# Optimization experiments

Measured on AMD Instinct MI355X. Metric: run time of the kernel, lower is better.

## Reference

```python
import jax, jax.numpy as jnp
import numpy as np

C = 512
C8 = C // 8
B, H, W = 4, 64, 64


def _conv1x1(x, w, b):
    # x: (B, Cin, H, W), w: (Cout, Cin), b: (Cout,)
    return jnp.einsum('oi,bihw->bohw', w, x) + b[None, :, None, None]


def setup_inputs() -> dict:
    key = jax.random.key(0)
    ks = jax.random.split(key, 16)
    s = 0.02
    inp = {
        'x': jax.random.normal(ks[0], (B, C, H, W), dtype=jnp.float32),
        'wpq': jax.random.normal(ks[1], (C8, C), dtype=jnp.float32) * s,
        'bpq': jnp.zeros((C8,), jnp.float32),
        'wpk': jax.random.normal(ks[2], (C8, C), dtype=jnp.float32) * s,
        'bpk': jnp.zeros((C8,), jnp.float32),
        'wpv': jax.random.normal(ks[3], (C, C), dtype=jnp.float32) * s,
        'bpv': jnp.zeros((C,), jnp.float32),
        'wcq': jax.random.normal(ks[4], (C, C), dtype=jnp.float32) * s,
        'bcq': jnp.zeros((C,), jnp.float32),
        'wck': jax.random.normal(ks[5], (C, C), dtype=jnp.float32) * s,
        'bck': jnp.zeros((C,), jnp.float32),
        'wcv': jax.random.normal(ks[6], (C, C), dtype=jnp.float32) * s,
        'bcv': jnp.zeros((C,), jnp.float32),
        # gammas are zero-init in torch; use small nonzero values so both
        # attention branches contribute to the output numerically.
        'gpos': jax.random.normal(ks[7], (1,), dtype=jnp.float32) * 0.1,
        'gchan': jax.random.normal(ks[8], (1,), dtype=jnp.float32) * 0.1,
    }
    return inp


def reference(x, wpq, bpq, wpk, bpk, wpv, bpv, wcq, bcq, wck, bck, wcv, bcv, gpos, gchan):
    b, c, h, w = x.shape
    n = h * w
    # ---- position attention ----
    pos_q = _conv1x1(x, wpq, bpq).reshape(b, C8, n)           # (b, C/8, N)
    pos_k = _conv1x1(x, wpk, bpk).reshape(b, C8, n)           # (b, C/8, N)
    pos_v = _conv1x1(x, wpv, bpv).reshape(b, c, n)            # (b, C, N)
    pos_attn = jax.nn.softmax(jnp.einsum('bcq,bck->bqk', pos_q, pos_k), axis=-1)  # (b, N, N)
    pos_out = jnp.einsum('bck,bqk->bcq', pos_v, pos_attn).reshape(b, c, h, w)
    pos_out = gpos * pos_out + x
    # ---- channel attention ----
    chan_q = _conv1x1(pos_out, wcq, bcq).reshape(b, c, n)
    chan_k = _conv1x1(pos_out, wck, bck).reshape(b, c, n)
    chan_v = _conv1x1(pos_out, wcv, bcv).reshape(b, c, n)
    chan_attn = jax.nn.softmax(jnp.einsum('bin,bjn->bij', chan_q, chan_k), axis=-1)  # (b, C, C)
    chan_out = jnp.einsum('bij,bjn->bin', chan_attn, chan_v).reshape(b, c, h, w)
    return gchan * chan_out + pos_out
```

## Files before the change

kernel.cpp:

```cpp
#include <hip/hip_runtime.h>
#include <hip/hip_bf16.h>
#include <math.h>

typedef __bf16 bf16;
typedef __attribute__((ext_vector_type(8))) __bf16 bf16x8;
typedef __attribute__((ext_vector_type(4))) __bf16 bf16x4;
typedef __attribute__((ext_vector_type(4))) float f32x4;

#define DEVI static __device__ __forceinline__

DEVI int swzb(int row, int ch) { return ((ch ^ (row & 7)) << 4); }

DEVI void gl_lds16(const void* g, void* l) {
  __builtin_amdgcn_global_load_lds(
      (const __attribute__((address_space(1))) unsigned int*)g,
      (__attribute__((address_space(3))) unsigned int*)l, 16, 0, 0);
}

__global__ __launch_bounds__(256) void prep_weights(
    const float* __restrict__ wpq, const float* __restrict__ wpk,
    const float* __restrict__ wpv, const float* __restrict__ wcq,
    const float* __restrict__ wck, const float* __restrict__ wcv,
    const float* __restrict__ bpq, const float* __restrict__ bpk,
    bf16* __restrict__ wqk, bf16* __restrict__ wpvb, bf16* __restrict__ wcqb,
    bf16* __restrict__ wckb, bf16* __restrict__ wcvT, float* __restrict__ bqk)
{
  int i = blockIdx.x * 256 + threadIdx.x;
  switch (blockIdx.y) {
    case 0: if (i < 64*512)  wqk[i]          = (bf16)wpq[i]; break;
    case 1: if (i < 64*512)  wqk[64*512 + i] = (bf16)wpk[i]; break;
    case 2: if (i < 512*512) wpvb[i] = (bf16)wpv[i]; break;
    case 3: if (i < 512*512) wcqb[i] = (bf16)wcq[i]; break;
    case 4: if (i < 512*512) wckb[i] = (bf16)wck[i]; break;
    case 5: if (i < 512*512) { int t = i >> 9, j = i & 511; wcvT[i] = (bf16)wcv[j*512 + t]; } break;
    case 6: if (i < 64) bqk[i] = bpq[i]; else if (i < 128) bqk[i] = bpk[i - 64]; break;
  }
}

__global__ __launch_bounds__(256) void transpose_x(const float* __restrict__ x, bf16* __restrict__ xbT)
{
  __shared__ float t[32][33];
  int b = blockIdx.z, n0 = blockIdx.x * 32, c0 = blockIdx.y * 32;
  int tx = threadIdx.x & 31, ty = threadIdx.x >> 5;
#pragma unroll
  for (int i = 0; i < 4; ++i)
    t[ty + 8*i][tx] = x[((size_t)b*512 + c0 + ty + 8*i)*4096 + n0 + tx];
  __syncthreads();
#pragma unroll
  for (int i = 0; i < 4; ++i)
    xbT[((size_t)b*4096 + n0 + ty + 8*i)*512 + c0 + tx] = (bf16)t[tx][ty + 8*i];
}

struct GemmP {
  const bf16* A; const bf16* Bt; void* C;
  long aS, bS;
  long cSbytes;
  int lda, ldb, ldc, K;
  const float* biasM; const float* biasN;
  const float* e_bq; const float* e_v; const float* e_u; const float* e_bk; float e_nn;
  long vS, uS;
  const float* gchan; const float* Abv; const bf16* Pres; long abvS, presS;
};

template<int BM, int BN, int BIAS, int EPI>
__global__ __launch_bounds__(256) void gemm_k(GemmP p)
{
  constexpr int QF = BM / 32;
  constexpr int CF = BN / 32;
  __shared__ __align__(16) char sa[2][BM * 128];
  __shared__ __align__(16) char sb[2][BN * 128];
  const int tid = threadIdx.x, lane = tid & 63, w = tid >> 6;
  const int g = lane >> 4, l15 = lane & 15;
  const int bm = blockIdx.x * BM, bn = blockIdx.y * BN, bz = blockIdx.z;
  const bf16* A  = p.A  + (size_t)bz * p.aS;
  const bf16* Bt = p.Bt + (size_t)bz * p.bS;
  char* Cb = (char*)p.C + (size_t)bz * p.cSbytes;
  const int wm = (w & 1) * (BM / 2), wn = (w >> 1) * (BN / 2);
  const int srow = tid >> 3, sch = tid & 7;

  f32x4 acc[QF][CF];
#pragma unroll
  for (int i = 0; i < QF; ++i)
#pragma unroll
    for (int j = 0; j < CF; ++j) acc[i][j] = f32x4{0.f, 0.f, 0.f, 0.f};

  auto stage = [&](int k0, int bi) {
#pragma unroll
    for (int it = 0; it < BM / 32; ++it) {
      int r = it * 32 + srow;
      gl_lds16(A + (size_t)(bm + r) * p.lda + k0 + ((sch ^ (r & 7)) * 8),
               sa[bi] + (it * 32 + w * 8) * 128);
    }
#pragma unroll
    for (int it = 0; it < BN / 32; ++it) {
      int r = it * 32 + srow;
      gl_lds16(Bt + (size_t)(bn + r) * p.ldb + k0 + ((sch ^ (r & 7)) * 8),
               sb[bi] + (it * 32 + w * 8) * 128);
    }
  };

  stage(0, 0);
  __syncthreads();
  const int nk = p.K >> 6;
  for (int t = 0; t < nk; ++t) {
    const int cur = t & 1;
    if (t + 1 < nk) stage((t + 1) << 6, cur ^ 1);
#pragma unroll
    for (int kc = 0; kc < 2; ++kc) {
      bf16x8 af[QF], bfr[CF];
#pragma unroll
      for (int qf = 0; qf < QF; ++qf) {
        int row = wm + 16 * qf + l15;
        af[qf] = *(const bf16x8*)(sa[cur] + row * 128 + swzb(row, g + 4 * kc));
      }
#pragma unroll
      for (int cf = 0; cf < CF; ++cf) {
        int row = wn + 16 * cf + l15;
        bfr[cf] = *(const bf16x8*)(sb[cur] + row * 128 + swzb(row, g + 4 * kc));
      }
      __builtin_amdgcn_s_setprio(1);
#pragma unroll
      for (int qf = 0; qf < QF; ++qf)
#pragma unroll
        for (int cf = 0; cf < CF; ++cf)
          acc[qf][cf] = __builtin_amdgcn_mfma_f32_16x16x32_bf16(af[qf], bfr[cf], acc[qf][cf], 0, 0, 0);
      __builtin_amdgcn_s_setprio(0);
    }
    __syncthreads();
  }

  float gc = 0.f;
  const float* AbvB = nullptr; const bf16* PresB = nullptr;
  const float* eV = nullptr; const float* eU = nullptr;
  if (EPI == 3) { gc = p.gchan[0]; AbvB = p.Abv + (size_t)bz * p.abvS; PresB = p.Pres + (size_t)bz * p.presS; }
  if (EPI == 2) { eV = p.e_v + (size_t)bz * p.vS; eU = p.e_u + (size_t)bz * p.uS; }

#pragma unroll
  for (int qf = 0; qf < QF; ++qf)
#pragma unroll
    for (int cf = 0; cf < CF; ++cf)
#pragma unroll
      for (int r = 0; r < 4; ++r) {
        int m = bm + wm + 16 * qf + 4 * g + r;
        int n = bn + wn + 16 * cf + l15;
        float v = acc[qf][cf][r];
        if (BIAS == 1) v += p.biasM[m];
        if (BIAS == 2) v += p.biasN[n];
        size_t idx = (size_t)m * p.ldc + n;
        if (EPI == 0) ((bf16*)Cb)[idx] = (bf16)v;
        else if (EPI == 1) ((float*)Cb)[idx] = v;
        else if (EPI == 2) {
          v += p.e_bq[m] * eV[n] + eU[m] * p.e_bk[n] + p.e_nn * p.e_bq[m] * p.e_bk[n];
          ((float*)Cb)[idx] = v;
        } else {
          v = gc * (v + AbvB[m]) + (float)PresB[idx];
          ((float*)Cb)[idx] = v;
        }
      }
}

__global__ __launch_bounds__(512, 4) void flash_pos(
    const bf16* __restrict__ QKT, const bf16* __restrict__ Vv,
    const float* __restrict__ x, const float* __restrict__ gpos,
    bf16* __restrict__ Pb, bf16* __restrict__ PTb)
{
  extern __shared__ char sm[];
  char* Plds = sm + 16384;
  float* Och  = (float*)sm;
  float* lsum = (float*)(sm + 34816);

  const int tid = threadIdx.x, lane = tid & 63, w = tid >> 6;
  const int g = lane >> 4, l15 = lane & 15;
  const int wq = w & 3;
  const int wh = w >> 2;
  const int phys = blockIdx.x;
  const int b  = (phys & 7) >> 1;
  const int ch = phys & 1;
  const int q0 = (phys >> 3) << 6;
  const int c0 = ch << 8;

  const bf16* QKTb = QKT + (size_t)b * 4096 * 128;
  const bf16* Vb   = Vv  + (size_t)b * 512 * 4096;

  const bf16* qrow = QKTb + (size_t)(q0 + 16 * wq + l15) * 128;
  bf16x8 qa0 = *(const bf16x8*)(qrow + 8 * g);
  bf16x8 qa1 = *(const bf16x8*)(qrow + 32 + 8 * g);

  f32x4 acc[4][2];
#pragma unroll
  for (int i = 0; i < 4; ++i) { acc[i][0] = f32x4{0.f,0.f,0.f,0.f}; acc[i][1] = f32x4{0.f,0.f,0.f,0.f}; }
  f32x4 l_r = f32x4{0.f, 0.f, 0.f, 0.f};

  const int srow = tid >> 3, sch = tid & 7;
  const bf16* Ksrc = QKTb + (size_t)srow * 128 + 64 + ((sch ^ (srow & 7)) * 8);
  const bf16* vb0 = Vb + (size_t)(c0 + 32 * w + l15) * 4096 + g * 8;
  const bf16* vb1 = vb0 + (size_t)16 * 4096;

  bf16x8 vA[2][2], vB[2][2];

  auto subiter = [&](const char* Kcur, char* Knext, int ktn,
                     bf16x8 (&vC)[2][2], bf16x8 (&vN)[2][2]) {
    gl_lds16(Ksrc + (size_t)ktn * 8192, Knext + w * 1024);
    __builtin_amdgcn_sched_barrier(0);
#pragma unroll
    for (int kc = 0; kc < 2; ++kc) {
      vN[kc][0] = *(const bf16x8*)(vb0 + ktn * 64 + kc * 32);
      vN[kc][1] = *(const bf16x8*)(vb1 + ktn * 64 + kc * 32);
    }
    f32x4 s0 = f32x4{0.f,0.f,0.f,0.f}, s1 = f32x4{0.f,0.f,0.f,0.f};
    {
      const int r0 = 32 * wh + l15, r1 = r0 + 16;
      bf16x8 k00 = *(const bf16x8*)(Kcur + r0 * 128 + swzb(r0, g));
      bf16x8 k01 = *(const bf16x8*)(Kcur + r0 * 128 + swzb(r0, g + 4));
      bf16x8 k10 = *(const bf16x8*)(Kcur + r1 * 128 + swzb(r1, g));
      bf16x8 k11 = *(const bf16x8*)(Kcur + r1 * 128 + swzb(r1, g + 4));
      s0 = __builtin_amdgcn_mfma_f32_16x16x32_bf16(qa0, k00, s0, 0, 0, 0);
      s0 = __builtin_amdgcn_mfma_f32_16x16x32_bf16(qa1, k01, s0, 0, 0, 0);
      s1 = __builtin_amdgcn_mfma_f32_16x16x32_bf16(qa0, k10, s1, 0, 0, 0);
      s1 = __builtin_amdgcn_mfma_f32_16x16x32_bf16(qa1, k11, s1, 0, 0, 0);
    }
#pragma unroll
    for (int r = 0; r < 4; ++r) {
      float e0 = __expf(s0[r]), e1 = __expf(s1[r]);
      l_r[r] += e0 + e1;
      int row = 16 * wq + 4 * g + r;
      int ca = 32 * wh + l15, cb = ca + 16;
      *(bf16*)(Plds + row * 128 + (((ca >> 3) ^ (row & 7)) << 4) + ((ca & 7) * 2)) = (bf16)e0;
      *(bf16*)(Plds + row * 128 + (((cb >> 3) ^ (row & 7)) << 4) + ((cb & 7) * 2)) = (bf16)e1;
    }
    asm volatile("s_waitcnt lgkmcnt(0)" ::: "memory");
    __builtin_amdgcn_sched_barrier(0);
    __builtin_amdgcn_s_barrier();
    __builtin_amdgcn_sched_barrier(0);
    __builtin_amdgcn_s_setprio(1);
#pragma unroll
    for (int kc = 0; kc < 2; ++kc)
#pragma unroll
      for (int qf = 0; qf < 4; ++qf) {
        int row = 16 * qf + l15;
        bf16x8 ap = *(const bf16x8*)(Plds + row * 128 + swzb(row, g + 4 * kc));
        acc[qf][0] = __builtin_amdgcn_mfma_f32_16x16x32_bf16(ap, vC[kc][0], acc[qf][0], 0, 0, 0);
        acc[qf][1] = __builtin_amdgcn_mfma_f32_16x16x32_bf16(ap, vC[kc][1], acc[qf][1], 0, 0, 0);
      }
    __builtin_amdgcn_s_setprio(0);
    asm volatile("s_waitcnt vmcnt(4) lgkmcnt(0)" ::: "memory");
    __builtin_amdgcn_sched_barrier(0);
    __builtin_amdgcn_s_barrier();
    __builtin_amdgcn_sched_barrier(0);
  };

  gl_lds16(Ksrc, sm + w * 1024);
  __builtin_amdgcn_sched_barrier(0);
#pragma unroll
  for (int kc = 0; kc < 2; ++kc) {
    vA[kc][0] = *(const bf16x8*)(vb0 + kc * 32);
    vA[kc][1] = *(const bf16x8*)(vb1 + kc * 32);
  }
  asm volatile("s_waitcnt vmcnt(4)" ::: "memory");
  __builtin_amdgcn_sched_barrier(0);
  __builtin_amdgcn_s_barrier();
  __builtin_amdgcn_sched_barrier(0);

  for (int t = 0; t < 64; t += 2) {
    subiter(sm,        sm + 8192, (t + 1) & 63, vA, vB);
    subiter(sm + 8192, sm,        (t + 2) & 63, vB, vA);
  }
  asm volatile("s_waitcnt vmcnt(0) lgkmcnt(0)" ::: "memory");
  __builtin_amdgcn_sched_barrier(0);
  __builtin_amdgcn_s_barrier();
  __builtin_amdgcn_sched_barrier(0);

#pragma unroll
  for (int off = 1; off < 16; off <<= 1) {
#pragma unroll
    for (int r = 0; r < 4; ++r) l_r[r] += __shfl_xor(l_r[r], off);
  }
  if (l15 == 0)
#pragma unroll
    for (int r = 0; r < 4; ++r) lsum[wh * 64 + 16 * wq + 4 * g + r] = l_r[r];
  __syncthreads();

  const float gp = gpos[0];
  for (int j = 0; j < 2; ++j) {
    if ((w >> 2) == j) {
#pragma unroll
      for (int qf = 0; qf < 4; ++qf) {
        float inv[4];
#pragma unroll
        for (int r = 0; r < 4; ++r) {
          int qi = 16 * qf + 4 * g + r;
          inv[r] = gp / (lsum[qi] + lsum[64 + qi]);
        }
#pragma unroll
        for (int cf = 0; cf < 2; ++cf) {
          int cl = 32 * (w & 3) + 16 * cf + l15;
#pragma unroll
          for (int r = 0; r < 4; ++r)
            Och[cl * 68 + 16 * qf + 4 * g + r] = acc[qf][cf][r] * inv[r];
        }
      }
    }
    __syncthreads();
    {
      int cl = tid >> 2, qs = (tid & 3) * 16;
      int cg = c0 + 128 * j + cl;
      const float* xr = x + ((size_t)b * 512 + cg) * 4096 + q0 + qs;
      float* och = Och + cl * 68 + qs;
      float tmp[16];
#pragma unroll
      for (int i = 0; i < 16; ++i) { tmp[i] = och[i] + xr[i]; och[i] = tmp[i]; }
      bf16x8 o0, o1;
#pragma unroll
      for (int i = 0; i < 8; ++i) { o0[i] = (bf16)tmp[i]; o1[i] = (bf16)tmp[i + 8]; }
      bf16* pr = Pb + ((size_t)b * 512 + cg) * 4096 + q0 + qs;
      *(bf16x8*)pr = o0; *(bf16x8*)(pr + 8) = o1;
    }
    __syncthreads();
    {
      int q = tid >> 3, cs = (tid & 7) * 16;
      float tmp[16];
#pragma unroll
      for (int i = 0; i < 16; ++i) tmp[i] = Och[(cs + i) * 68 + q];
      bf16x8 o0, o1;
#pragma unroll
      for (int i = 0; i < 8; ++i) { o0[i] = (bf16)tmp[i]; o1[i] = (bf16)tmp[i + 8]; }
      bf16* pt = PTb + ((size_t)b * 4096 + q0 + q) * 512 + c0 + 128 * j + cs;
      *(bf16x8*)pt = o0; *(bf16x8*)(pt + 8) = o1;
    }
    __syncthreads();
  }
}

__global__ __launch_bounds__(256) void row_sum(const bf16* __restrict__ Pb, float* __restrict__ r)
{
  int wid = blockIdx.x * 4 + (threadIdx.x >> 6);
  int lane = threadIdx.x & 63;
  const bf16* row = Pb + (size_t)wid * 4096;
  float s = 0.f;
#pragma unroll
  for (int i = 0; i < 8; ++i) {
    bf16x8 v = ((const bf16x8*)row)[lane + 64 * i];
#pragma unroll
    for (int j = 0; j < 8; ++j) s += (float)v[j];
  }
#pragma unroll
  for (int off = 1; off < 64; off <<= 1) s += __shfl_xor(s, off);
  if (lane == 0) r[wid] = s;
}

__global__ __launch_bounds__(256) void uv_kernel(
    const float* __restrict__ wcq, const float* __restrict__ wck,
    const float* __restrict__ r, float* __restrict__ u, float* __restrict__ v)
{
  int b = blockIdx.z;
  int i = blockIdx.x * 256 + threadIdx.x;
  const float* rb = r + b * 512;
  const float* wrow = (blockIdx.y ? wck : wcq) + (size_t)i * 512;
  float s = 0.f;
  for (int t = 0; t < 512; ++t) s += wrow[t] * rb[t];
  (blockIdx.y ? v : u)[b * 512 + i] = s;
}

__global__ __launch_bounds__(256) void softmax_chan(
    const float* __restrict__ L, const float* __restrict__ bcv,
    bf16* __restrict__ Ab, float* __restrict__ Abv)
{
  int b = blockIdx.z;
  int i = blockIdx.x * 4 + (threadIdx.x >> 6);
  int lane = threadIdx.x & 63;
  const float* row = L + ((size_t)b * 512 + i) * 512;
  f32x4 v0 = ((const f32x4*)row)[lane];
  f32x4 v1 = ((const f32x4*)row)[lane + 64];
  float mx = fmaxf(fmaxf(fmaxf(v0[0], v0[1]), fmaxf(v0[2], v0[3])),
                   fmaxf(fmaxf(v1[0], v1[1]), fmaxf(v1[2], v1[3])));
#pragma unroll
  for (int off = 1; off < 64; off <<= 1) mx = fmaxf(mx, __shfl_xor(mx, off));
  float e[8]; float s = 0.f;
#pragma unroll
  for (int k = 0; k < 4; ++k) { e[k] = __expf(v0[k] - mx); s += e[k]; }
#pragma unroll
  for (int k = 0; k < 4; ++k) { e[4 + k] = __expf(v1[k] - mx); s += e[4 + k]; }
#pragma unroll
  for (int off = 1; off < 64; off <<= 1) s += __shfl_xor(s, off);
  float inv = 1.f / s;
  bf16x4 a0, a1;
  const f32x4 bv0 = ((const f32x4*)bcv)[lane];
  const f32x4 bv1 = ((const f32x4*)bcv)[lane + 64];
  float pb = 0.f;
#pragma unroll
  for (int k = 0; k < 4; ++k) {
    float p0 = e[k] * inv, p1 = e[4 + k] * inv;
    a0[k] = (bf16)p0; a1[k] = (bf16)p1;
    pb += p0 * bv0[k] + p1 * bv1[k];
  }
  bf16* arow = Ab + ((size_t)b * 512 + i) * 512;
  *(bf16x4*)(arow + 4 * lane) = a0;
  *(bf16x4*)(arow + 256 + 4 * lane) = a1;
#pragma unroll
  for (int off = 1; off < 64; off <<= 1) pb += __shfl_xor(pb, off);
  if (lane == 0) Abv[b * 512 + i] = pb;
}

extern "C" void kernel_launch(void* const* d_in, const int* in_sizes, int n_in,
                              void* d_out, int out_size, void* d_ws, size_t ws_size,
                              hipStream_t stream)
{
  const float* x    = (const float*)d_in[0];
  const float* wpq  = (const float*)d_in[1];
  const float* bpq  = (const float*)d_in[2];
  const float* wpk  = (const float*)d_in[3];
  const float* bpk  = (const float*)d_in[4];
  const float* wpv  = (const float*)d_in[5];
  const float* bpv  = (const float*)d_in[6];
  const float* wcq  = (const float*)d_in[7];
  const float* bcq  = (const float*)d_in[8];
  const float* wck  = (const float*)d_in[9];
  const float* bck  = (const float*)d_in[10];
  const float* wcv  = (const float*)d_in[11];
  const float* bcv  = (const float*)d_in[12];
  const float* gpos = (const float*)d_in[13];
  const float* gch  = (const float*)d_in[14];
  float* out = (float*)d_out;

  char* ws = (char*)d_ws;
  size_t off = 0;
  auto alloc = [&](size_t bytes) -> char* {
    char* p = ws + off; off = (off + bytes + 255) & ~(size_t)255; return p;
  };
  bf16*  xbT  = (bf16*)alloc(4UL * 4096 * 512 * 2);
  bf16*  QKT  = (bf16*)alloc(4UL * 4096 * 128 * 2);
  bf16*  V    = (bf16*)alloc(4UL * 512 * 4096 * 2);
  bf16*  Pb   = (bf16*)alloc(4UL * 512 * 4096 * 2);
  bf16*  PTb  = (bf16*)alloc(4UL * 4096 * 512 * 2);
  bf16*  G    = (bf16*)alloc(4UL * 512 * 512 * 2);
  bf16*  M1   = (bf16*)alloc(4UL * 512 * 512 * 2);
  float* Lws  = (float*)alloc(4UL * 512 * 512 * 4);
  bf16*  Ab   = (bf16*)alloc(4UL * 512 * 512 * 2);
  bf16*  B2   = (bf16*)alloc(4UL * 512 * 512 * 2);
  bf16*  wqk  = (bf16*)alloc(128UL * 512 * 2);
  bf16*  wpvb = (bf16*)alloc(512UL * 512 * 2);
  bf16*  wcqb = (bf16*)alloc(512UL * 512 * 2);
  bf16*  wckb = (bf16*)alloc(512UL * 512 * 2);
  bf16*  wcvT = (bf16*)alloc(512UL * 512 * 2);
  float* bqk  = (float*)alloc(128 * 4);
  float* rws  = (float*)alloc(4UL * 512 * 4);
  float* uws  = (float*)alloc(4UL * 512 * 4);
  float* vws  = (float*)alloc(4UL * 512 * 4);
  float* Abv  = (float*)alloc(4UL * 512 * 4);
  if (off > ws_size) return;

  prep_weights<<<dim3(1024, 7, 1), 256, 0, stream>>>(wpq, wpk, wpv, wcq, wck, wcv,
                                                     bpq, bpk, wqk, wpvb, wcqb, wckb, wcvT, bqk);
  transpose_x<<<dim3(128, 16, 4), 256, 0, stream>>>(x, xbT);

  GemmP p{};
  p = GemmP{};
  p.A = xbT; p.aS = 4096L * 512; p.lda = 512;
  p.Bt = wqk; p.bS = 0; p.ldb = 512;
  p.C = QKT; p.cSbytes = 4096L * 128 * 2; p.ldc = 128;
  p.K = 512; p.biasN = bqk;
  gemm_k<128, 64, 2, 0><<<dim3(32, 2, 4), 256, 0, stream>>>(p);

  p = GemmP{};
  p.A = wpvb; p.aS = 0; p.lda = 512;
  p.Bt = xbT; p.bS = 4096L * 512; p.ldb = 512;
  p.C = V; p.cSbytes = 512L * 4096 * 2; p.ldc = 4096;
  p.K = 512; p.biasM = bpv;
  gemm_k<128, 128, 1, 0><<<dim3(4, 32, 4), 256, 0, stream>>>(p);

  flash_pos<<<dim3(512, 1, 1), 512, 35328, stream>>>(QKT, V, x, gpos, Pb, PTb);

  p = GemmP{};
  p.A = Pb; p.aS = 512L * 4096; p.lda = 4096;
  p.Bt = Pb; p.bS = 512L * 4096; p.ldb = 4096;
  p.C = G; p.cSbytes = 512L * 512 * 2; p.ldc = 512;
  p.K = 4096;
  gemm_k<64, 64, 0, 0><<<dim3(8, 8, 4), 256, 0, stream>>>(p);

  row_sum<<<dim3(512, 1, 1), 256, 0, stream>>>(Pb, rws);
  uv_kernel<<<dim3(2, 2, 4), 256, 0, stream>>>(wcq, wck, rws, uws, vws);

  p = GemmP{};
  p.A = wcqb; p.aS = 0; p.lda = 512;
  p.Bt = G; p.bS = 512L * 512; p.ldb = 512;
  p.C = M1; p.cSbytes = 512L * 512 * 2; p.ldc = 512;
  p.K = 512;
  gemm_k<64, 64, 0, 0><<<dim3(8, 8, 4), 256, 0, stream>>>(p);

  p = GemmP{};
  p.A = M1; p.aS = 512L * 512; p.lda = 512;
  p.Bt = wckb; p.bS = 0; p.ldb = 512;
  p.C = Lws; p.cSbytes = 512L * 512 * 4; p.ldc = 512;
  p.K = 512;
  p.e_bq = bcq; p.e_v = vws; p.vS = 512; p.e_u = uws; p.uS = 512; p.e_bk = bck; p.e_nn = 4096.f;
  gemm_k<64, 64, 0, 2><<<dim3(8, 8, 4), 256, 0, stream>>>(p);

  softmax_chan<<<dim3(128, 1, 4), 256, 0, stream>>>(Lws, bcv, Ab, Abv);

  p = GemmP{};
  p.A = Ab; p.aS = 512L * 512; p.lda = 512;
  p.Bt = wcvT; p.bS = 0; p.ldb = 512;
  p.C = B2; p.cSbytes = 512L * 512 * 2; p.ldc = 512;
  p.K = 512;
  gemm_k<64, 64, 0, 0><<<dim3(8, 8, 4), 256, 0, stream>>>(p);

  p = GemmP{};
  p.A = B2; p.aS = 512L * 512; p.lda = 512;
  p.Bt = PTb; p.bS = 4096L * 512; p.ldb = 512;
  p.C = out; p.cSbytes = 512L * 4096 * 4; p.ldc = 4096;
  p.K = 512;
  p.gchan = gch; p.Abv = Abv; p.abvS = 512; p.Pres = Pb; p.presS = 512L * 4096;
  gemm_k<128, 128, 0, 3><<<dim3(4, 32, 4), 256, 0, stream>>>(p);
}
```

Baseline: 303.0 us.

## Triple-buffer GEMM staging and double-buffer P tile in flash_pos

The GEMM kernel moves to a three-stage LDS ring for small tiles (BM+BN<=192). It prefetches two K-steps ahead and waits on explicit vmcnt counts, so only one barrier is needed per iteration. In flash_pos the P tile now alternates between two LDS buffers keyed to the K buffer, which removes one of the two barriers per sub-iteration. This cuts synchronisation stalls but uses more LDS, which may lower occupancy. It also depends on the vmcnt counts being exact for correctness.

New measurement: 304.2 us. No clear change (+0.4%).

```diff
diff --git a/kernel.cpp b/kernel.cpp
--- a/kernel.cpp
+++ b/kernel.cpp
@@ -15,6 +15,18 @@
   __builtin_amdgcn_global_load_lds(
       (const __attribute__((address_space(1))) unsigned int*)g,
       (__attribute__((address_space(3))) unsigned int*)l, 16, 0, 0);
+}
+
+template<int N> DEVI void wait_vm() {
+  if constexpr (N == 0) asm volatile("s_waitcnt vmcnt(0)" ::: "memory");
+  else if constexpr (N == 4) asm volatile("s_waitcnt vmcnt(4)" ::: "memory");
+  else if constexpr (N == 6) asm volatile("s_waitcnt vmcnt(6)" ::: "memory");
+  else if constexpr (N == 8) asm volatile("s_waitcnt vmcnt(8)" ::: "memory");
+}
+DEVI void sbar() {
+  __builtin_amdgcn_sched_barrier(0);
+  __builtin_amdgcn_s_barrier();
+  __builtin_amdgcn_sched_barrier(0);
 }
 
 __global__ __launch_bounds__(256) void prep_weights(
@@ -67,8 +79,10 @@
 {
   constexpr int QF = BM / 32;
   constexpr int CF = BN / 32;
-  __shared__ __align__(16) char sa[2][BM * 128];
-  __shared__ __align__(16) char sb[2][BN * 128];
+  constexpr int NBUF = (BM + BN <= 192) ? 3 : 2;
+  constexpr int LOADS = (BM + BN) / 32;
+  __shared__ __align__(16) char sa[NBUF][BM * 128];
+  __shared__ __align__(16) char sb[NBUF][BN * 128];
   const int tid = threadIdx.x, lane = tid & 63, w = tid >> 6;
   const int g = lane >> 4, l15 = lane & 15;
   const int bm = blockIdx.x * BM, bn = blockIdx.y * BN, bz = blockIdx.z;
@@ -98,25 +112,19 @@
                sb[bi] + (it * 32 + w * 8) * 128);
     }
   };
-
-  stage(0, 0);
-  __syncthreads();
-  const int nk = p.K >> 6;
-  for (int t = 0; t < nk; ++t) {
-    const int cur = t & 1;
-    if (t + 1 < nk) stage((t + 1) << 6, cur ^ 1);
+  auto compute = [&](int bi) {
 #pragma unroll
     for (int kc = 0; kc < 2; ++kc) {
       bf16x8 af[QF], bfr[CF];
 #pragma unroll
       for (int qf = 0; qf < QF; ++qf) {
         int row = wm + 16 * qf + l15;
-        af[qf] = *(const bf16x8*)(sa[cur] + row * 128 + swzb(row, g + 4 * kc));
+        af[qf] = *(const bf16x8*)(sa[bi] + row * 128 + swzb(row, g + 4 * kc));
       }
 #pragma unroll
       for (int cf = 0; cf < CF; ++cf) {
         int row = wn + 16 * cf + l15;
-        bfr[cf] = *(const bf16x8*)(sb[cur] + row * 128 + swzb(row, g + 4 * kc));
+        bfr[cf] = *(const bf16x8*)(sb[bi] + row * 128 + swzb(row, g + 4 * kc));
       }
       __builtin_amdgcn_s_setprio(1);
 #pragma unroll
@@ -126,7 +134,33 @@
           acc[qf][cf] = __builtin_amdgcn_mfma_f32_16x16x32_bf16(af[qf], bfr[cf], acc[qf][cf], 0, 0, 0);
       __builtin_amdgcn_s_setprio(0);
     }
+  };
+
+  const int nk = p.K >> 6;
+  if constexpr (NBUF == 3) {
+    stage(0, 0);
+    if (nk > 1) { stage(64, 1); wait_vm<LOADS>(); } else wait_vm<0>();
+    sbar();
+    int bi = 0;
+    for (int t = 0; t < nk; ++t) {
+      int b2 = bi + 2; if (b2 >= 3) b2 -= 3;
+      if (t + 2 < nk) stage((t + 2) << 6, b2);
+      compute(bi);
+      if (t + 1 < nk) {
+        if (t + 2 < nk) wait_vm<LOADS>(); else wait_vm<0>();
+        sbar();
+      }
+      if (++bi == 3) bi = 0;
+    }
+  } else {
+    stage(0, 0);
     __syncthreads();
+    for (int t = 0; t < nk; ++t) {
+      const int cur = t & 1;
+      if (t + 1 < nk) stage((t + 1) << 6, cur ^ 1);
+      compute(cur);
+      __syncthreads();
+    }
   }
 
   float gc = 0.f;
@@ -165,7 +199,6 @@
     bf16* __restrict__ Pb, bf16* __restrict__ PTb)
 {
   extern __shared__ char sm[];
-  char* Plds = sm + 16384;
   float* Och  = (float*)sm;
   float* lsum = (float*)(sm + 34816);
 
@@ -198,8 +231,10 @@
 
   bf16x8 vA[2][2], vB[2][2];
 
-  auto subiter = [&](const char* Kcur, char* Knext, int ktn,
-                     bf16x8 (&vC)[2][2], bf16x8 (&vN)[2][2]) {
+  auto subiter = [&](int koff, int ktn, bf16x8 (&vC)[2][2], bf16x8 (&vN)[2][2]) {
+    char* Kcur = sm + koff;
+    char* Knext = sm + (koff ^ 8192);
+    char* Pcur = sm + 16384 + koff;
     gl_lds16(Ksrc + (size_t)ktn * 8192, Knext + w * 1024);
     __builtin_amdgcn_sched_barrier(0);
 #pragma unroll
@@ -225,28 +260,22 @@
       l_r[r] += e0 + e1;
       int row = 16 * wq + 4 * g + r;
       int ca = 32 * wh + l15, cb = ca + 16;
-      *(bf16*)(Plds + row * 128 + (((ca >> 3) ^ (row & 7)) << 4) + ((ca & 7) * 2)) = (bf16)e0;
-      *(bf16*)(Plds + row * 128 + (((cb >> 3) ^ (row & 7)) << 4) + ((cb & 7) * 2)) = (bf16)e1;
-    }
-    asm volatile("s_waitcnt lgkmcnt(0)" ::: "memory");
-    __builtin_amdgcn_sched_barrier(0);
-    __builtin_amdgcn_s_barrier();
-    __builtin_amdgcn_sched_barrier(0);
+      *(bf16*)(Pcur + row * 128 + (((ca >> 3) ^ (row & 7)) << 4) + ((ca & 7) * 2)) = (bf16)e0;
+      *(bf16*)(Pcur + row * 128 + (((cb >> 3) ^ (row & 7)) << 4) + ((cb & 7) * 2)) = (bf16)e1;
+    }
+    asm volatile("s_waitcnt vmcnt(4) lgkmcnt(0)" ::: "memory");
+    sbar();
     __builtin_amdgcn_s_setprio(1);
 #pragma unroll
     for (int kc = 0; kc < 2; ++kc)
 #pragma unroll
       for (int qf = 0; qf < 4; ++qf) {
         int row = 16 * qf + l15;
-        bf16x8 ap = *(const bf16x8*)(Plds + row * 128 + swzb(row, g + 4 * kc));
+        bf16x8 ap = *(const bf16x8*)(Pcur + row * 128 + swzb(row, g + 4 * kc));
         acc[qf][0] = __builtin_amdgcn_mfma_f32_16x16x32_bf16(ap, vC[kc][0], acc[qf][0], 0, 0, 0);
         acc[qf][1] = __builtin_amdgcn_mfma_f32_16x16x32_bf16(ap, vC[kc][1], acc[qf][1], 0, 0, 0);
       }
     __builtin_amdgcn_s_setprio(0);
-    asm volatile("s_waitcnt vmcnt(4) lgkmcnt(0)" ::: "memory");
-    __builtin_amdgcn_sched_barrier(0);
-    __builtin_amdgcn_s_barrier();
-    __builtin_amdgcn_sched_barrier(0);
   };
 
   gl_lds16(Ksrc, sm + w * 1024);
@@ -257,18 +286,14 @@
     vA[kc][1] = *(const bf16x8*)(vb1 + kc * 32);
   }
   asm volatile("s_waitcnt vmcnt(4)" ::: "memory");
-  __builtin_amdgcn_sched_barrier(0);
-  __builtin_amdgcn_s_barrier();
-  __builtin_amdgcn_sched_barrier(0);
+  sbar();
 
   for (int t = 0; t < 64; t += 2) {
-    subiter(sm,        sm + 8192, (t + 1) & 63, vA, vB);
-    subiter(sm + 8192, sm,        (t + 2) & 63, vB, vA);
+    subiter(0,    (t + 1) & 63, vA, vB);
+    subiter(8192, (t + 2) & 63, vB, vA);
   }
   asm volatile("s_waitcnt vmcnt(0) lgkmcnt(0)" ::: "memory");
-  __builtin_amdgcn_sched_barrier(0);
-  __builtin_amdgcn_s_barrier();
-  __builtin_amdgcn_sched_barrier(0);
+  sbar();
 
 #pragma unroll
   for (int off = 1; off < 16; off <<= 1) {
```
